# Kernel tuning notes

Hardware: AMD Instinct MI355X
Metric: run time of the kernel (lower is better)

The kernel has to match this reference:

```python
import jax, jax.numpy as jnp
import numpy as np

D = 256; NHEAD = 8; NQ = 300; NLAYERS = 6; NLEV = 3; NPTS = 4
DFF = 1024; NCLS = 80; BS = 16
SPATIAL = ((80, 80), (40, 40), (20, 20))
LM = sum(h * w for h, w in SPATIAL)
DH = D // NHEAD
PARAM_NAMES = ['sa_wq','sa_bq','sa_wk','sa_bk','sa_wv','sa_bv','sa_wo','sa_bo',
               'ln1_g','ln1_b','ln2_g','ln2_b','ln3_g','ln3_b',
               'off_w','off_b','attw_w','attw_b','val_w','val_b','out_w','out_b',
               'ffn_w1','ffn_b1','ffn_w2','ffn_b2',
               'bb_w1','bb_b1','bb_w2','bb_b2','bb_w3','bb_b3',
               'sc_w','sc_b','qp_w1','qp_b1','qp_w2','qp_b2']


def _ln(x, g, b, eps=1e-5):
    m = x.mean(-1, keepdims=True)
    v = ((x - m) ** 2).mean(-1, keepdims=True)
    return (x - m) * jax.lax.rsqrt(v + eps) * g + b


def _mlp2(x, w1, b1, w2, b2):
    # 2-layer MLP, ReLU on hidden only (act_final_layer=False)
    return jnp.maximum(x @ w1 + b1, 0.0) @ w2 + b2


def _inv_sigmoid(x, eps=1e-5):
    x = jnp.clip(x, 0.0, 1.0)
    return jnp.log(jnp.clip(x, eps, None) / jnp.clip(1.0 - x, eps, None))


def _mha(q, k, v, wq, bq, wk, bk, wv, bv, wo, bo):
    B, N, _ = q.shape
    Q = (q @ wq + bq).reshape(B, N, NHEAD, DH)
    K = (k @ wk + bk).reshape(B, N, NHEAD, DH)
    V = (v @ wv + bv).reshape(B, N, NHEAD, DH)
    att = jnp.einsum('bqhd,bkhd->bhqk', Q, K) * (1.0 / np.sqrt(DH))
    att = jax.nn.softmax(att, axis=-1)
    o = jnp.einsum('bhqk,bkhd->bqhd', att, V).reshape(B, N, D)
    return o @ wo + bo


def _bilinear(v, x, y, Hl, Wl):
    # v: [B, Hl*Wl, C]; x, y: [B, M] pixel coords (align_corners=False, zero padding)
    x0 = jnp.floor(x); y0 = jnp.floor(y)
    wx = x - x0; wy = y - y0
    out = 0.0
    for dx, dy, w in ((0, 0, (1 - wx) * (1 - wy)), (1, 0, wx * (1 - wy)),
                      (0, 1, (1 - wx) * wy), (1, 1, wx * wy)):
        xi = x0 + dx; yi = y0 + dy
        valid = (xi >= 0) & (xi < Wl) & (yi >= 0) & (yi < Hl)
        lin = (jnp.clip(yi, 0, Hl - 1) * Wl + jnp.clip(xi, 0, Wl - 1)).astype(jnp.int32)
        g = jnp.take_along_axis(v, lin[..., None], axis=1)
        out = out + g * (w * valid)[..., None]
    return out


def _deform_attn(q, ref, memory, ow, ob, aw, ab, vw, vb, pw, pb):
    # q: [B,NQ,D]; ref: [B,NQ,4] cxcywh in [0,1]; memory: [B,LM,D]
    B = q.shape[0]
    value = (memory @ vw + vb).reshape(B, LM, NHEAD, DH)
    off = (q @ ow + ob).reshape(B, NQ, NHEAD, NLEV, NPTS, 2)
    attw = jax.nn.softmax((q @ aw + ab).reshape(B, NQ, NHEAD, NLEV * NPTS), -1)
    attw = attw.reshape(B, NQ, NHEAD, NLEV, NPTS)
    r = ref[:, :, None, None, None, :]
    loc = r[..., :2] + off / NPTS * r[..., 2:] * 0.5  # [B,NQ,H,LV,P,2]
    start = 0
    acc = 0.0
    for lv, (Hl, Wl) in enumerate(SPATIAL):
        v = value[:, start:start + Hl * Wl]  # [B, Hl*Wl, H, DH]
        v = v.transpose(0, 2, 1, 3).reshape(B * NHEAD, Hl * Wl, DH)
        g = loc[:, :, :, lv]  # [B,NQ,H,P,2]
        x = (g[..., 0] * Wl - 0.5).transpose(0, 2, 1, 3).reshape(B * NHEAD, NQ * NPTS)
        y = (g[..., 1] * Hl - 0.5).transpose(0, 2, 1, 3).reshape(B * NHEAD, NQ * NPTS)
        s = _bilinear(v, x, y, Hl, Wl).reshape(B, NHEAD, NQ, NPTS, DH)
        w = attw[:, :, :, lv].transpose(0, 2, 1, 3)  # [B,H,NQ,P]
        acc = acc + (s * w[..., None]).sum(3)  # [B,H,NQ,DH]
        start += Hl * Wl
    o = acc.transpose(0, 2, 1, 3).reshape(B, NQ, D)
    return o @ pw + pb


def _decoder(tgt, ref_points_unact, memory, p):
    ref_d = jax.nn.sigmoid(ref_points_unact)
    out = tgt
    for i in range(NLAYERS):
        pos = _mlp2(ref_d, p['qp_w1'], p['qp_b1'], p['qp_w2'], p['qp_b2'])
        q = out + pos
        t2 = _mha(q, q, out, p['sa_wq'][i], p['sa_bq'][i], p['sa_wk'][i], p['sa_bk'][i],
                  p['sa_wv'][i], p['sa_bv'][i], p['sa_wo'][i], p['sa_bo'][i])
        out = _ln(out + t2, p['ln1_g'][i], p['ln1_b'][i])
        t2 = _deform_attn(out + pos, ref_d, memory, p['off_w'][i], p['off_b'][i],
                          p['attw_w'][i], p['attw_b'][i], p['val_w'][i], p['val_b'][i],
                          p['out_w'][i], p['out_b'][i])
        out = _ln(out + t2, p['ln2_g'][i], p['ln2_b'][i])
        out = _ln(out + _mlp2(out, p['ffn_w1'][i], p['ffn_b1'][i], p['ffn_w2'][i], p['ffn_b2'][i]),
                  p['ln3_g'][i], p['ln3_b'][i])
        h = jnp.maximum(out @ p['bb_w1'][i] + p['bb_b1'][i], 0.0)
        h = jnp.maximum(h @ p['bb_w2'][i] + p['bb_b2'][i], 0.0)
        delta = h @ p['bb_w3'][i] + p['bb_b3'][i]
        ref_d = jax.nn.sigmoid(delta + _inv_sigmoid(ref_d))
    logits = out @ p['sc_w'][NLAYERS - 1] + p['sc_b'][NLAYERS - 1]
    return ref_d, logits


def setup_inputs():
    key = jax.random.key(0)
    keys = iter(jax.random.split(key, 64))
    def rn(shape, s=0.02):
        return jax.random.normal(next(keys), shape, jnp.float32) * s
    L = NLAYERS
    inp = {
        'tgt': rn((BS, NQ, D), 1.0),
        'ref_points_unact': rn((BS, NQ, 4), 1.0),
        'memory': rn((BS, LM, D), 1.0),
    }
    for n in ['sa_wq', 'sa_wk', 'sa_wv', 'sa_wo', 'val_w', 'out_w', 'bb_w1', 'bb_w2']:
        inp[n] = rn((L, D, D))
    for n in ['sa_bq', 'sa_bk', 'sa_bv', 'sa_bo', 'ln1_b', 'ln2_b', 'ln3_b',
              'val_b', 'out_b', 'ffn_b2', 'bb_b1', 'bb_b2']:
        inp[n] = jnp.zeros((L, D), jnp.float32)
    for n in ['ln1_g', 'ln2_g', 'ln3_g']:
        inp[n] = jnp.ones((L, D), jnp.float32)
    OFF = NHEAD * NLEV * NPTS * 2
    ATT = NHEAD * NLEV * NPTS
    inp['off_w'] = rn((L, D, OFF)); inp['off_b'] = rn((L, OFF), 0.1)
    inp['attw_w'] = rn((L, D, ATT)); inp['attw_b'] = jnp.zeros((L, ATT), jnp.float32)
    inp['ffn_w1'] = rn((L, D, DFF)); inp['ffn_b1'] = jnp.zeros((L, DFF), jnp.float32)
    inp['ffn_w2'] = rn((L, DFF, D))
    inp['bb_w3'] = rn((L, D, 4)); inp['bb_b3'] = jnp.zeros((L, 4), jnp.float32)
    inp['sc_w'] = rn((L, D, NCLS)); inp['sc_b'] = jnp.zeros((L, NCLS), jnp.float32)
    inp['qp_w1'] = rn((4, 2 * D)); inp['qp_b1'] = jnp.zeros((2 * D,), jnp.float32)
    inp['qp_w2'] = rn((2 * D, D)); inp['qp_b2'] = jnp.zeros((D,), jnp.float32)
    return inp


def reference(tgt, ref_points_unact, memory, sa_wq, sa_bq, sa_wk, sa_bk, sa_wv, sa_bv,
              sa_wo, sa_bo, ln1_g, ln1_b, ln2_g, ln2_b, ln3_g, ln3_b, off_w, off_b,
              attw_w, attw_b, val_w, val_b, out_w, out_b, ffn_w1, ffn_b1, ffn_w2, ffn_b2,
              bb_w1, bb_b1, bb_w2, bb_b2, bb_w3, bb_b3, sc_w, sc_b,
              qp_w1, qp_b1, qp_w2, qp_b2):
    _a = dict(locals())
    p = {k: _a[k] for k in PARAM_NAMES}
    ref_d, logits = _decoder(tgt, ref_points_unact, memory, p)
    # eval path: stacked final-layer outputs, shape [1, BS, NQ, 4] and [1, BS, NQ, NCLS]
    return ref_d[None], logits[None]
```

## Files before the change

kernel.cpp:

```cpp
#include <hip/hip_runtime.h>
#include <hip/hip_bf16.h>

typedef __hip_bfloat16 bf16;
typedef short short8 __attribute__((ext_vector_type(8)));
typedef short short4v __attribute__((ext_vector_type(4)));
typedef float float4v __attribute__((ext_vector_type(4)));

#define D_ 256
#define NHEAD_ 8
#define DH_ 32
#define NQ_ 300
#define NLAYERS_ 6
#define DFF_ 1024
#define NCLS_ 80
#define BS_ 16
#define LM_ 8400
#define BN_ (BS_*NQ_)

static __device__ __forceinline__ short f2bf(float x){
    union{float f; unsigned u;} v; v.f = x;
    unsigned r = v.u + 0x7FFF + ((v.u>>16)&1);
    return (short)(r>>16);
}
static __device__ __forceinline__ float bf2f(short s){
    union{unsigned u; float f;} v; v.u = ((unsigned)(unsigned short)s)<<16; return v.f;
}

__global__ __launch_bounds__(256) void valproj_kernel(
    const short* __restrict__ memT, const short* __restrict__ WTall, size_t zWT,
    const float* __restrict__ vb, short* __restrict__ values)
{
    int m0 = blockIdx.x*64;
    int tid = threadIdx.x, lane = tid&63, wave = tid>>6;
    int wm = (wave>>1)*32, wn = (wave&1)*32;
    int lr = lane&15, lq = lane>>4;
    short8 af[2][8];
    #pragma unroll
    for(int t=0;t<8;t++){
        #pragma unroll
        for(int mi=0;mi<2;mi++)
            af[mi][t] = *(const short8*)(memT + (size_t)(m0+wm+mi*16+lr)*256 + t*32 + lq*8);
    }
    short8 pb[2][2];
    #pragma unroll
    for(int ni=0;ni<2;ni++)
        pb[0][ni] = *(const short8*)(WTall + (size_t)(wn+ni*16+lr)*256 + lq*8);
    for(int c=0;c<24;c++){
        int zi = c>>2;
        int n0 = (c&3)*64;
        float4v acc[2][2];
        #pragma unroll
        for(int i=0;i<2;i++)
            #pragma unroll
            for(int j=0;j<2;j++){ acc[i][j].x=0.f; acc[i][j].y=0.f; acc[i][j].z=0.f; acc[i][j].w=0.f; }
        const short* wz = WTall + (size_t)zi*zWT;
        #pragma unroll
        for(int t=0;t<8;t++){
            const int cur = t&1;
            if(t<7){
                #pragma unroll
                for(int ni=0;ni<2;ni++)
                    pb[cur^1][ni] = *(const short8*)(wz + (size_t)(n0+wn+ni*16+lr)*256 + (t+1)*32 + lq*8);
            } else if(c<23){
                int c2 = c+1; int zi2 = c2>>2; int n02 = (c2&3)*64;
                const short* wz2 = WTall + (size_t)zi2*zWT;
                #pragma unroll
                for(int ni=0;ni<2;ni++)
                    pb[cur^1][ni] = *(const short8*)(wz2 + (size_t)(n02+wn+ni*16+lr)*256 + lq*8);
            }
            acc[0][0] = __builtin_amdgcn_mfma_f32_16x16x32_bf16(af[0][t], pb[cur][0], acc[0][0], 0,0,0);
            acc[0][1] = __builtin_amdgcn_mfma_f32_16x16x32_bf16(af[0][t], pb[cur][1], acc[0][1], 0,0,0);
            acc[1][0] = __builtin_amdgcn_mfma_f32_16x16x32_bf16(af[1][t], pb[cur][0], acc[1][0], 0,0,0);
            acc[1][1] = __builtin_amdgcn_mfma_f32_16x16x32_bf16(af[1][t], pb[cur][1], acc[1][1], 0,0,0);
        }
        const float* bb = vb + (size_t)zi*256;
        bf16* out = (bf16*)values + (size_t)zi*((size_t)134400*256);
        #pragma unroll
        for(int mi=0;mi<2;mi++){
            #pragma unroll
            for(int rr=0;rr<4;rr++){
                int gm = m0+wm+mi*16+lq*4+rr;
                #pragma unroll
                for(int ni=0;ni<2;ni++){
                    int gn = n0+wn+ni*16+lr;
                    out[(size_t)gm*256+gn] = __float2bfloat16(acc[mi][ni][rr]+bb[gn]);
                }
            }
        }
    }
}

__global__ __launch_bounds__(256) void pos_mlp_kernel(
    const float* __restrict__ refd, const float* __restrict__ w1, const float* __restrict__ b1,
    const short* __restrict__ w2T, const float* __restrict__ b2, float* __restrict__ pos)
{
    __shared__ short hs[32*520];
    __shared__ float rs[32*4];
    int n0 = blockIdx.x*64, m0 = blockIdx.y*32;
    int tid = threadIdx.x;
    if(tid<128) rs[tid] = refd[(size_t)m0*4 + tid];
    __syncthreads();
    {
        int c0 = tid&255;
        float w1r[2][4], b1r[2];
        #pragma unroll
        for(int h=0;h<2;h++){
            int c = c0 + h*256;
            b1r[h] = b1[c];
            #pragma unroll
            for(int k=0;k<4;k++) w1r[h][k] = w1[k*512+c];
        }
        #pragma unroll 4
        for(int j=0;j<64;j++){
            int r = j>>1, h = j&1;
            int c = c0 + h*256;
            float v = 0.f;
            #pragma unroll
            for(int k=0;k<4;k++) v = fmaf(rs[r*4+k], w1r[h][k], v);
            v += b1r[h];
            hs[r*520+c] = f2bf(fmaxf(v,0.f));
        }
    }
    __syncthreads();
    int lane = tid&63, wave = tid>>6;
    int wm = (wave>>1)*16, wn = (wave&1)*32;
    int lr = lane&15, lq = lane>>4;
    float4v acc[2];
    #pragma unroll
    for(int j=0;j<2;j++){ acc[j].x=0.f; acc[j].y=0.f; acc[j].z=0.f; acc[j].w=0.f; }
    short8 pb[2][2];
    #pragma unroll
    for(int ni=0;ni<2;ni++)
        pb[0][ni] = *(const short8*)(w2T + (size_t)(n0+wn+ni*16+lr)*512 + lq*8);
    #pragma unroll
    for(int t=0;t<16;t++){
        const int cur = t&1;
        if(t<15){
            #pragma unroll
            for(int ni=0;ni<2;ni++)
                pb[cur^1][ni] = *(const short8*)(w2T + (size_t)(n0+wn+ni*16+lr)*512 + (t+1)*32 + lq*8);
        }
        short8 a0 = *(const short8*)(&hs[(wm+lr)*520 + t*32 + lq*8]);
        acc[0] = __builtin_amdgcn_mfma_f32_16x16x32_bf16(a0, pb[cur][0], acc[0], 0,0,0);
        acc[1] = __builtin_amdgcn_mfma_f32_16x16x32_bf16(a0, pb[cur][1], acc[1], 0,0,0);
    }
    #pragma unroll
    for(int rr=0;rr<4;rr++){
        int gm = m0+wm+lq*4+rr;
        #pragma unroll
        for(int ni=0;ni<2;ni++){
            int gn = n0+wn+ni*16+lr;
            pos[(size_t)gm*256+gn] = acc[ni][rr] + b2[gn];
        }
    }
}

#define LSTR 40

template<int TM, int TN, bool ABF16, bool RELU, bool OUTBF16>
__global__ __launch_bounds__(256) void mfma_gemm_kernel(
    const void* __restrict__ Av, const void* __restrict__ A2v,
    const void* __restrict__ A3v, int nA2lim,
    const short* __restrict__ WT, size_t zWT,
    const float* __restrict__ b0, const float* __restrict__ b1,
    const float* __restrict__ b2, int ns1, int ns2, size_t zB,
    void* __restrict__ Cv, size_t zC, int M, int K, int N, int nxt)
{
    __shared__ short As[2][TM*LSTR];
    __shared__ short Bs[2][TN*LSTR];
    int zz, n0;
    if(nxt){ zz = blockIdx.x / nxt; n0 = (blockIdx.x % nxt)*TN; }
    else   { zz = blockIdx.z;       n0 = blockIdx.x*TN; }
    WT += (size_t)zz*zWT; b0 += (size_t)zz*zB; b1 += (size_t)zz*zB; b2 += (size_t)zz*zB;
    int tid = threadIdx.x;
    int lane = tid&63, wave = tid>>6;
    int m0 = blockIdx.y*TM;
    const int MI = TM/32;
    const int NI = TN/32;
    int wm = (wave>>1)*(TM/2), wn = (wave&1)*(TN/2);
    int lr = lane&15, lq = lane>>4;
    float4v acc[MI][NI];
    #pragma unroll
    for(int i=0;i<MI;i++)
        #pragma unroll
        for(int j=0;j<NI;j++){ acc[i][j].x=0.f; acc[i][j].y=0.f; acc[i][j].z=0.f; acc[i][j].w=0.f; }

    const float* Af; const float* Ad; const short* Ah;
    if(ABF16){ Ah = (const short*)Av; Af=nullptr; Ad=nullptr; }
    else {
        Af = (n0 < nA2lim)? (const float*)Av : (const float*)A3v;
        Ad = (n0 < nA2lim)? (const float*)A2v : nullptr;
        Ah = nullptr;
    }

    short8  rA16[ABF16? TM/64 : 1];
    float4v rAf [ABF16? 1 : TM/32];
    float4v rAd [ABF16? 1 : TM/32];
    short8  rB[TN/64];

    auto LOAD = [&](int k0){
        if constexpr(ABF16){
            #pragma unroll
            for(int it=0; it<TM/64; ++it){
                int idx=(it*256+tid)*8; int r=idx>>5, kk=idx&31; int gm=m0+r;
                short8 v = {};
                if(gm<M) v = *(const short8*)(Ah + (size_t)gm*K + (k0+kk));
                rA16[it]=v;
            }
        } else {
            #pragma unroll
            for(int it=0; it<TM/32; ++it){
                int idx=(it*256+tid)*4; int r=idx>>5, kk=idx&31; int gm=m0+r;
                float4v v; v.x=0.f;v.y=0.f;v.z=0.f;v.w=0.f;
                float4v w; w.x=0.f;w.y=0.f;w.z=0.f;w.w=0.f;
                if(gm<M){
                    v = *(const float4v*)(Af + (size_t)gm*K + (k0+kk));
                    if(Ad) w = *(const float4v*)(Ad + (size_t)gm*K + (k0+kk));
                }
                rAf[it]=v; rAd[it]=w;
            }
        }
        #pragma unroll
        for(int it=0; it<TN/64; ++it){
            int idx=(it*256+tid)*8; int r=idx>>5, kk=idx&31; int gn=n0+r;
            short8 v = {};
            if(gn<N) v = *(const short8*)(WT + (size_t)gn*K + (k0+kk));
            rB[it]=v;
        }
    };
    auto STORE = [&](int buf){
        if constexpr(ABF16){
            #pragma unroll
            for(int it=0; it<TM/64; ++it){
                int idx=(it*256+tid)*8; int r=idx>>5, kk=idx&31;
                *(short8*)(&As[buf][r*LSTR+kk]) = rA16[it];
            }
        } else {
            #pragma unroll
            for(int it=0; it<TM/32; ++it){
                int idx=(it*256+tid)*4; int r=idx>>5, kk=idx&31;
                float4v v = rAf[it];
                if(Ad){ v.x+=rAd[it].x; v.y+=rAd[it].y; v.z+=rAd[it].z; v.w+=rAd[it].w; }
                short4v h; h.x=f2bf(v.x); h.y=f2bf(v.y); h.z=f2bf(v.z); h.w=f2bf(v.w);
                *(short4v*)(&As[buf][r*LSTR+kk]) = h;
            }
        }
        #pragma unroll
        for(int it=0; it<TN/64; ++it){
            int idx=(it*256+tid)*8; int r=idx>>5, kk=idx&31;
            *(short8*)(&Bs[buf][r*LSTR+kk]) = rB[it];
        }
    };

    const int nt = K>>5;
    LOAD(0);
    STORE(0);
    __syncthreads();
    for(int t=0; t<nt; ++t){
        int cb = t&1;
        if(t+1<nt) LOAD((t+1)<<5);
        short8 af[MI], bfr[NI];
        #pragma unroll
        for(int mi=0;mi<MI;mi++) af[mi]  = *(const short8*)(&As[cb][(wm+mi*16+lr)*LSTR + lq*8]);
        #pragma unroll
        for(int ni=0;ni<NI;ni++) bfr[ni] = *(const short8*)(&Bs[cb][(wn+ni*16+lr)*LSTR + lq*8]);
        #pragma unroll
        for(int mi=0;mi<MI;mi++)
            #pragma unroll
            for(int ni=0;ni<NI;ni++)
                acc[mi][ni] = __builtin_amdgcn_mfma_f32_16x16x32_bf16(af[mi], bfr[ni], acc[mi][ni], 0,0,0);
        if(t+1<nt){
            STORE(cb^1);
            __syncthreads();
        }
    }
    float* Cf=(float*)Cv + (size_t)zz*zC; bf16* Ch=(bf16*)Cv + (size_t)zz*zC;
    #pragma unroll
    for(int mi=0;mi<MI;mi++){
        #pragma unroll
        for(int r=0;r<4;r++){
            int gm = m0+wm+mi*16+lq*4+r;
            if(gm>=M) continue;
            #pragma unroll
            for(int ni=0;ni<NI;ni++){
                int gn = n0+wn+ni*16+lr;
                if(gn>=N) continue;
                float bv = (gn<ns1)? b0[gn] : ((gn<ns2)? b1[gn-ns1] : b2[gn-ns2]);
                float v = acc[mi][ni][r] + bv;
                if(RELU) v = fmaxf(v,0.f);
                if(OUTBF16) Ch[(size_t)gm*N+gn]=__float2bfloat16(v);
                else        Cf[(size_t)gm*N+gn]=v;
            }
        }
    }
}

__global__ __launch_bounds__(256) void fused_mha_kernel(
    const float* __restrict__ QKV, short* __restrict__ O)
{
    const int ld = 768;
    int bh = blockIdx.y; int b = bh>>3, h = bh&7;
    int q0 = blockIdx.x*64;
    __shared__ short lds[31104];
    short* Vts = lds;
    short* Qs  = lds + 10368;
    short* Ks  = lds + 12672;
    short* Ps  = lds + 10368;
    int tid = threadIdx.x;
    for(int idx=tid; idx<64*8; idx+=256){
        int r=idx>>3, c4=(idx&7)*4; int gq=q0+r;
        float4v v; v.x=0.f;v.y=0.f;v.z=0.f;v.w=0.f;
        if(gq<NQ_) v = *(const float4v*)(QKV + ((size_t)(b*NQ_+gq))*ld + h*DH_ + c4);
        short4v h4; h4.x=f2bf(v.x);h4.y=f2bf(v.y);h4.z=f2bf(v.z);h4.w=f2bf(v.w);
        *(short4v*)(Qs + r*36 + c4) = h4;
    }
    for(int idx=tid; idx<304*8; idx+=256){
        int r=idx>>3, c4=(idx&7)*4;
        float4v v; v.x=0.f;v.y=0.f;v.z=0.f;v.w=0.f;
        if(r<NQ_) v = *(const float4v*)(QKV + 256 + ((size_t)(b*NQ_+r))*ld + h*DH_ + c4);
        short4v h4; h4.x=f2bf(v.x);h4.y=f2bf(v.y);h4.z=f2bf(v.z);h4.w=f2bf(v.w);
        *(short4v*)(Ks + r*36 + c4) = h4;
    }
    for(int idx=tid; idx<320*8; idx+=256){
        int r=idx>>3, c4=(idx&7)*4;
        float4v v; v.x=0.f;v.y=0.f;v.z=0.f;v.w=0.f;
        if(r<NQ_) v = *(const float4v*)(QKV + 512 + ((size_t)(b*NQ_+r))*ld + h*DH_ + c4);
        Vts[(c4+0)*324+r]=f2bf(v.x); Vts[(c4+1)*324+r]=f2bf(v.y);
        Vts[(c4+2)*324+r]=f2bf(v.z); Vts[(c4+3)*324+r]=f2bf(v.w);
    }
    __syncthreads();

    int lane = tid&63, wave = tid>>6;
    int lr = lane&15, lq = lane>>4;
    int mrow = wave*16;
    const float scale = 0.17677669529663687f;

    float4v acc[19];
    #pragma unroll
    for(int t=0;t<19;t++){ acc[t].x=0.f; acc[t].y=0.f; acc[t].z=0.f; acc[t].w=0.f; }
    short8 afrag = *(const short8*)(&Qs[(mrow+lr)*36 + lq*8]);
    #pragma unroll
    for(int t=0;t<19;t++){
        short8 bfrag = *(const short8*)(&Ks[(t*16+lr)*36 + lq*8]);
        acc[t] = __builtin_amdgcn_mfma_f32_16x16x32_bf16(afrag, bfrag, acc[t], 0,0,0);
    }
    __syncthreads();

    for(int idx=tid; idx<64*16; idx+=256){
        int r=idx>>4, c=idx&15;
        Ps[r*324 + 304 + c]=0;
    }
    #pragma unroll
    for(int t=0;t<19;t++){
        #pragma unroll
        for(int r=0;r<4;r++) acc[t][r] *= scale;
    }
    if(lr>=12){
        #pragma unroll
        for(int r=0;r<4;r++) acc[18][r] = -1e30f;
    }
    float mx[4];
    #pragma unroll
    for(int r=0;r<4;r++){
        float m = acc[0][r];
        #pragma unroll
        for(int t=1;t<19;t++) m = fmaxf(m, acc[t][r]);
        m = fmaxf(m, __shfl_xor(m,1)); m = fmaxf(m, __shfl_xor(m,2));
        m = fmaxf(m, __shfl_xor(m,4)); m = fmaxf(m, __shfl_xor(m,8));
        mx[r]=m;
    }
    float sum[4] = {0.f,0.f,0.f,0.f};
    #pragma unroll
    for(int t=0;t<19;t++){
        #pragma unroll
        for(int r=0;r<4;r++){
            float p = __expf(acc[t][r]-mx[r]);
            acc[t][r]=p; sum[r]+=p;
        }
    }
    #pragma unroll
    for(int r=0;r<4;r++){
        float s = sum[r];
        s += __shfl_xor(s,1); s += __shfl_xor(s,2);
        s += __shfl_xor(s,4); s += __shfl_xor(s,8);
        sum[r] = 1.f/s;
    }
    #pragma unroll
    for(int t=0;t<19;t++){
        #pragma unroll
        for(int r=0;r<4;r++){
            Ps[(mrow + lq*4 + r)*324 + t*16 + lr] = f2bf(acc[t][r]*sum[r]);
        }
    }
    __syncthreads();
    float4v oacc[2];
    oacc[0].x=0.f;oacc[0].y=0.f;oacc[0].z=0.f;oacc[0].w=0.f;
    oacc[1]=oacc[0];
    #pragma unroll
    for(int kc=0;kc<10;kc++){
        short8 pa = *(const short8*)(&Ps[(mrow+lr)*324 + kc*32 + lq*8]);
        #pragma unroll
        for(int n=0;n<2;n++){
            short8 vb = *(const short8*)(&Vts[(n*16+lr)*324 + kc*32 + lq*8]);
            oacc[n] = __builtin_amdgcn_mfma_f32_16x16x32_bf16(pa, vb, oacc[n], 0,0,0);
        }
    }
    #pragma unroll
    for(int n=0;n<2;n++){
        #pragma unroll
        for(int r=0;r<4;r++){
            int gq = q0 + mrow + lq*4 + r;
            if(gq<NQ_)
                O[((size_t)(b*NQ_+gq))*D_ + h*DH_ + n*16 + lr] = f2bf(oacc[n][r]);
        }
    }
}

#define NTD 74
struct TD { const float* src; unsigned dstoff; int K, N, base; };
struct TAll { TD d[NTD]; };

__global__ __launch_bounds__(256) void transpose_all_kernel(TAll p, short* __restrict__ WTb){
    int blk = blockIdx.x;
    int di = 0;
    #pragma unroll 1
    for(int i=0;i<NTD;i++){ if(blk >= p.d[i].base) di = i; }
    TD d = p.d[di];
    int rel = blk - d.base;
    int ntx = (d.N+31)/32;
    int tn = (rel % ntx)*32, tk = (rel / ntx)*32;
    __shared__ float t[32][33];
    int tx = threadIdx.x&31, ty = threadIdx.x>>5;
    for(int i=0;i<32;i+=8){
        int k = tk+ty+i, n = tn+tx;
        t[ty+i][tx] = (k<d.K && n<d.N)? d.src[(size_t)k*d.N+n] : 0.f;
    }
    __syncthreads();
    short* out = WTb + d.dstoff;
    for(int i=0;i<32;i+=8){
        int n = tn+ty+i, k = tk+tx;
        if(n<d.N && k<d.K) out[(size_t)n*d.K+k] = f2bf(t[tx][ty+i]);
    }
}

template<bool RELU, bool BBOX>
__global__ __launch_bounds__(256) void gemm_kernel(
    const float* __restrict__ A, const float* __restrict__ W,
    const float* __restrict__ bias, float* __restrict__ Cf,
    int M, int K, int N)
{
    __shared__ float As[16][68];
    __shared__ float Bs[16][68];
    int tid = threadIdx.x;
    int m0 = blockIdx.y*64, n0 = blockIdx.x*64;
    int tm = tid>>4, tn = tid&15;
    float acc[4][4] = {};
    int lam = tid>>2;
    int lak = (tid&3)*4;
    int lbk = tid>>4;
    int lbn = (tid&15)*4;
    for(int k0=0;k0<K;k0+=16){
        {
            int m = m0+lam;
            #pragma unroll
            for(int j=0;j<4;j++){
                int k = k0+lak+j;
                float v=0.f;
                if(m<M && k<K) v = A[(size_t)m*K+k];
                As[lak+j][lam]=v;
            }
        }
        {
            int k = k0+lbk;
            #pragma unroll
            for(int j=0;j<4;j++){
                int n = n0+lbn+j;
                float v=0.f;
                if(k<K && n<N) v = W[(size_t)k*N+n];
                Bs[lbk][lbn+j]=v;
            }
        }
        __syncthreads();
        #pragma unroll
        for(int kk=0;kk<16;kk++){
            float a[4], bb[4];
            #pragma unroll
            for(int i=0;i<4;i++) a[i]=As[kk][tm*4+i];
            #pragma unroll
            for(int j=0;j<4;j++) bb[j]=Bs[kk][tn*4+j];
            #pragma unroll
            for(int i=0;i<4;i++)
                #pragma unroll
                for(int j=0;j<4;j++) acc[i][j] += a[i]*bb[j];
        }
        __syncthreads();
    }
    #pragma unroll
    for(int i=0;i<4;i++){
        int m=m0+tm*4+i; if(m>=M) continue;
        #pragma unroll
        for(int j=0;j<4;j++){
            int n=n0+tn*4+j; if(n>=N) continue;
            float v = acc[i][j] + bias[n];
            if(BBOX){
                float x = Cf[(size_t)m*N+n];
                x = fminf(fmaxf(x,0.f),1.f);
                float num = fmaxf(x,1e-5f), den = fmaxf(1.f-x,1e-5f);
                float nd = v + logf(num/den);
                Cf[(size_t)m*N+n] = 1.f/(1.f+expf(-nd));
            } else {
                if(RELU) v = fmaxf(v,0.f);
                Cf[(size_t)m*N+n]=v;
            }
        }
    }
}

__global__ void copy_kernel(const float* __restrict__ a, float* __restrict__ o, int n){
    int i = blockIdx.x*blockDim.x+threadIdx.x;
    if(i<n) o[i]=a[i];
}
__global__ void cvt_f32_bf16_kernel(const float* __restrict__ a, short* __restrict__ o, int n4){
    int i = blockIdx.x*blockDim.x+threadIdx.x;
    if(i<n4){
        float4v v = *(const float4v*)(a + (size_t)i*4);
        short4v h; h.x=f2bf(v.x); h.y=f2bf(v.y); h.z=f2bf(v.z); h.w=f2bf(v.w);
        *(short4v*)(o + (size_t)i*4) = h;
    }
}
__global__ void sigmoid_init_kernel(const float* __restrict__ a, float* __restrict__ o, int n){
    int i = blockIdx.x*blockDim.x+threadIdx.x;
    if(i<n){ float x=a[i]; o[i]=1.f/(1.f+expf(-x)); }
}
__global__ void write_out_kernel(const float* __restrict__ refd, const float* __restrict__ logits, float* __restrict__ out){
    int i = blockIdx.x*blockDim.x+threadIdx.x;
    if(i<BN_*4) out[i]=refd[i];
    else if(i<BN_*4+BN_*NCLS_) out[i]=logits[i-BN_*4];
}

__global__ __launch_bounds__(256) void ln_residual_kernel(
    float* __restrict__ cur, const short* __restrict__ t2b,
    const float* __restrict__ g, const float* __restrict__ b,
    short* __restrict__ cb)
{
    int row = blockIdx.x; int c = threadIdx.x;
    size_t idx = (size_t)row*D_+c;
    float x = cur[idx] + bf2f(t2b[idx]);
    float v1 = x, v2 = x*x;
    #pragma unroll
    for(int o=32;o>0;o>>=1){ v1 += __shfl_down(v1,o,64); v2 += __shfl_down(v2,o,64); }
    __shared__ float s1[4], s2[4], st[2];
    int wid=c>>6, lane=c&63;
    if(lane==0){ s1[wid]=v1; s2[wid]=v2; }
    __syncthreads();
    if(c==0){
        float a=0,d=0;
        #pragma unroll
        for(int i=0;i<4;i++){a+=s1[i]; d+=s2[i];}
        st[0]=a/(float)D_; st[1]=d/(float)D_;
    }
    __syncthreads();
    float m=st[0], var=st[1]-m*m;
    float y = (x-m)*rsqrtf(var+1e-5f)*g[c] + b[c];
    cur[idx]=y;
    if(cb) cb[idx]=f2bf(y);
}

__global__ __launch_bounds__(256) void deform_sample_kernel(
    const float* __restrict__ refd, const float* __restrict__ oab,
    const bf16* __restrict__ value, short* __restrict__ outacc)
{
    int row = blockIdx.x; int b = row/NQ_;
    int tid = threadIdx.x; int h = tid>>5, c = tid&31;
    __shared__ float so[192], sa[96], sr[4];
    if(tid<192) so[tid]=oab[(size_t)row*288+tid];
    if(tid<96)  sa[tid]=oab[(size_t)row*288+192+tid];
    if(tid<4)   sr[tid]=refd[(size_t)row*4+tid];
    __syncthreads();
    if(tid<8){
        float* p = sa + tid*12;
        float m=-1e30f;
        #pragma unroll
        for(int i2=0;i2<12;i2++) m=fmaxf(m,p[i2]);
        float s=0.f;
        #pragma unroll
        for(int i2=0;i2<12;i2++){ float e=__expf(p[i2]-m); p[i2]=e; s+=e; }
        float inv=1.f/s;
        #pragma unroll
        for(int i2=0;i2<12;i2++) p[i2]*=inv;
    }
    __syncthreads();
    float cx=sr[0], cy=sr[1], rw=sr[2], rh=sr[3];
    const int HS[3]={80,40,20}, WS[3]={80,40,20}, ST[3]={0,6400,8000};
    float acc=0.f;
    const bf16* vb = value + (size_t)b*LM_*D_ + h*DH_ + c;
    for(int lv=0;lv<3;lv++){
        int Hl=HS[lv], Wl=WS[lv], st=ST[lv];
        #pragma unroll
        for(int pt=0;pt<4;pt++){
            int oi = ((h*3+lv)*4+pt)*2;
            float ox=so[oi], oy=so[oi+1];
            float wa=sa[h*12+lv*4+pt];
            float lx = cx + ox*0.25f*rw*0.5f;
            float ly = cy + oy*0.25f*rh*0.5f;
            float x = lx*(float)Wl - 0.5f, y = ly*(float)Hl - 0.5f;
            float x0f=floorf(x), y0f=floorf(y);
            float wx=x-x0f, wy=y-y0f;
            int x0=(int)x0f, y0=(int)y0f;
            #pragma unroll
            for(int dy=0;dy<2;dy++){
                #pragma unroll
                for(int dx=0;dx<2;dx++){
                    int xi=x0+dx, yi=y0+dy;
                    if(xi>=0 && xi<Wl && yi>=0 && yi<Hl){
                        float w = (dx? wx : 1.f-wx)*(dy? wy : 1.f-wy);
                        int lin = yi*Wl+xi;
                        acc += __bfloat162float(vb[(size_t)(st+lin)*D_]) * (w*wa);
                    }
                }
            }
        }
    }
    outacc[(size_t)row*D_+tid]=f2bf(acc);
}

static void gemm_bbox(const float*A, const float*W, const float*b, float*refd,
                      int M,int K,int N, hipStream_t s){
    dim3 g((N+63)/64,(M+63)/64);
    gemm_kernel<false,true><<<g,256,0,s>>>(A,W,b,refd,M,K,N);
}
static void g64x(const void*A, const void*A2, const void*A3, int nA2lim,
                 const short*WT, const float*b0, const float*b1, const float*b2,
                 int ns1, int ns2, void*C, int M,int K,int N,
                 bool abf16, bool relu, bool outbf, hipStream_t s){
    dim3 g((N+63)/64,(M+63)/64,1);
    #define CALLG(AB,RL,OB) mfma_gemm_kernel<64,64,AB,RL,OB><<<g,256,0,s>>>(A,A2,A3,nA2lim,WT,0,b0,b1,b2,ns1,ns2,0,C,0,M,K,N,0)
    if(abf16){
        if(relu){ if(outbf) CALLG(true,true,true);  else CALLG(true,true,false); }
        else    { if(outbf) CALLG(true,false,true); else CALLG(true,false,false); }
    } else {
        if(relu){ if(outbf) CALLG(false,true,true);  else CALLG(false,true,false); }
        else    { if(outbf) CALLG(false,false,true); else CALLG(false,false,false); }
    }
    #undef CALLG
}
static void g64(const float*A, const float*A2, const float*A3, int nA2lim,
                const short*WT, const float*b0, const float*b1, const float*b2,
                int ns1, int ns2, void*C, int M,int K,int N,
                bool relu, bool outbf, hipStream_t s){
    g64x(A,A2,A3,nA2lim,WT,b0,b1,b2,ns1,ns2,C,M,K,N,false,relu,outbf,s);
}
static void g64b(const short*A, const short*WT, const float*b, void*C,
                 int M,int K,int N, hipStream_t s){
    g64x(A,nullptr,nullptr,1<<30,WT,b,b,b,N,N+1,C,M,K,N,true,false,true,s);
}
static int ntiles(int K,int N){ return ((N+31)/32)*((K+31)/32); }

extern "C" void kernel_launch(void* const* d_in, const int* in_sizes, int n_in,
                              void* d_out, int out_size, void* d_ws, size_t ws_size,
                              hipStream_t stream) {
    const float* tgt   = (const float*)d_in[0];
    const float* rpu   = (const float*)d_in[1];
    const float* mem   = (const float*)d_in[2];
    const float* sa_wq = (const float*)d_in[3];
    const float* sa_wk = (const float*)d_in[4];
    const float* sa_wv = (const float*)d_in[5];
    const float* sa_wo = (const float*)d_in[6];
    const float* val_w = (const float*)d_in[7];
    const float* out_w = (const float*)d_in[8];
    const float* bb_w1 = (const float*)d_in[9];
    const float* bb_w2 = (const float*)d_in[10];
    const float* sa_bq = (const float*)d_in[11];
    const float* sa_bk = (const float*)d_in[12];
    const float* sa_bv = (const float*)d_in[13];
    const float* sa_bo = (const float*)d_in[14];
    const float* ln1_b = (const float*)d_in[15];
    const float* ln2_b = (const float*)d_in[16];
    const float* ln3_b = (const float*)d_in[17];
    const float* val_b = (const float*)d_in[18];
    const float* out_b = (const float*)d_in[19];
    const float* ffn_b2= (const float*)d_in[20];
    const float* bb_b1 = (const float*)d_in[21];
    const float* bb_b2 = (const float*)d_in[22];
    const float* ln1_g = (const float*)d_in[23];
    const float* ln2_g = (const float*)d_in[24];
    const float* ln3_g = (const float*)d_in[25];
    const float* off_w = (const float*)d_in[26];
    const float* off_b = (const float*)d_in[27];
    const float* attw_w= (const float*)d_in[28];
    const float* attw_b= (const float*)d_in[29];
    const float* ffn_w1= (const float*)d_in[30];
    const float* ffn_b1= (const float*)d_in[31];
    const float* ffn_w2= (const float*)d_in[32];
    const float* bb_w3 = (const float*)d_in[33];
    const float* bb_b3 = (const float*)d_in[34];
    const float* sc_w  = (const float*)d_in[35];
    const float* sc_b  = (const float*)d_in[36];
    const float* qp_w1 = (const float*)d_in[37];
    const float* qp_b1 = (const float*)d_in[38];
    const float* qp_w2 = (const float*)d_in[39];
    const float* qp_b2 = (const float*)d_in[40];

    const size_t BND = (size_t)BN_*D_;
    const size_t USZ = (size_t)BN_*DFF_;
    const size_t LMD = (size_t)BS_*LM_*D_;
    const size_t LSZ = 1122304;

    float* ws   = (float*)d_ws;
    float* cur  = ws;
    float* pos  = cur + BND;
    float* refd = pos + BND;
    float* U    = refd + (size_t)BN_*4;
    short* tmp16 = (short*)(U + USZ);
    short* t216  = tmp16 + BND;
    short* WT    = t216 + BND;
    short* qp2T  = WT + 6*LSZ;
    short* scT   = qp2T + 131072;
    short* X     = scT + 20480;
    float* QKVh   = U;
    float* offsb  = U;
    short* ffnh16 = (short*)U;
    short* bb1b   = (short*)U;
    float* bb2    = U + BND;
    float* logitsb= U;
    short* curb = tmp16;

    size_t offX = (size_t)((char*)X - (char*)d_ws);
    int vmode;
    if(ws_size >= offX + 7*LMD*2)      vmode = 3;
    else if(ws_size >= offX + 6*LMD*2) vmode = 2;
    else if(ws_size >= offX + 4*LMD)   vmode = 1;
    else                               vmode = 0;
    short* memT   = X;
    short* values = (vmode==3)? X + LMD : X;
    short* value1 = X + LMD;
    short* value0 = X;

    const int nBN_D = (int)BND;
    copy_kernel<<<(nBN_D+255)/256,256,0,stream>>>(tgt, cur, nBN_D);
    sigmoid_init_kernel<<<(BN_*4+255)/256,256,0,stream>>>(rpu, refd, BN_*4);
    if(vmode==1 || vmode==3){
        int n4 = (int)(LMD/4);
        cvt_f32_bf16_kernel<<<(n4+255)/256,256,0,stream>>>(mem, memT, n4);
    }

    {
        TAll tp; int base=0; int di=0;
        const size_t offs[12] = { 0,65536,131072,196608,262144,327680,
                                  393216,442368,466944,729088,991232,1056768 };
        const int Ks[12] = { 256,256,256,256,256,256,256,256,256,1024,256,256 };
        const int Ns[12] = { 256,256,256,256,256,256,192,96,1024,256,256,256 };
        for(int l=0;l<NLAYERS_;l++){
            const float* srcs[12] = { sa_wq+(size_t)l*D_*D_, sa_wk+(size_t)l*D_*D_, sa_wv+(size_t)l*D_*D_,
                                      sa_wo+(size_t)l*D_*D_, val_w+(size_t)l*D_*D_, out_w+(size_t)l*D_*D_,
                                      off_w+(size_t)l*D_*192, attw_w+(size_t)l*D_*96,
                                      ffn_w1+(size_t)l*D_*DFF_, ffn_w2+(size_t)l*DFF_*D_,
                                      bb_w1+(size_t)l*D_*D_, bb_w2+(size_t)l*D_*D_ };
            for(int j=0;j<12;j++){
                tp.d[di] = { srcs[j], (unsigned)(l*LSZ + offs[j]), Ks[j], Ns[j], base };
                base += ntiles(Ks[j],Ns[j]); di++;
            }
        }
        tp.d[di] = { qp_w2, (unsigned)(6*LSZ), 512, 256, base }; base += ntiles(512,256); di++;
        tp.d[di] = { sc_w + (size_t)(NLAYERS_-1)*D_*NCLS_, (unsigned)(6*LSZ+131072), 256, 80, base }; base += ntiles(256,80); di++;
        transpose_all_kernel<<<base,256,0,stream>>>(tp, WT);
    }

    if(vmode==3){
        valproj_kernel<<<2100,256,0,stream>>>(memT, WT+262144, LSZ, val_b, values);
    } else if(vmode==2){
        dim3 g(12,1050,1);
        mfma_gemm_kernel<128,128,false,false,true><<<g,256,0,stream>>>(
            mem,nullptr,mem,1<<30, WT+262144, LSZ,
            val_b,val_b,val_b, 256,257, 256, values, LMD, BS_*LM_, D_, D_, 2);
    }

    for(int i=0;i<NLAYERS_;i++){
        const bf16* value_i;
        if(vmode>=2) value_i = (const bf16*)(values + (size_t)i*LMD);
        else {
            dim3 g(2,1050,1);
            if(vmode==1){
                mfma_gemm_kernel<128,128,true,false,true><<<g,256,0,stream>>>(
                    memT,nullptr,nullptr,1<<30, WT+i*LSZ+262144, 0,
                    val_b+(size_t)i*D_,val_b,val_b, 256,257, 0, value1, 0, BS_*LM_, D_, D_, 0);
                value_i = (const bf16*)value1;
            } else {
                mfma_gemm_kernel<128,128,false,false,true><<<g,256,0,stream>>>(
                    mem,nullptr,mem,1<<30, WT+i*LSZ+262144, 0,
                    val_b+(size_t)i*D_,val_b,val_b, 256,257, 0, value0, 0, BS_*LM_, D_, D_, 0);
                value_i = (const bf16*)value0;
            }
        }
        pos_mlp_kernel<<<dim3(4,150),256,0,stream>>>(refd, qp_w1, qp_b1, qp2T, qp_b2, pos);
        g64(cur, pos, cur, 512, WT+i*LSZ,
            sa_bq+(size_t)i*D_, sa_bk+(size_t)i*D_, sa_bv+(size_t)i*D_, 256, 512,
            QKVh, BN_, D_, 768, false,false, stream);
        {
            dim3 g((NQ_+63)/64, BS_*NHEAD_);
            fused_mha_kernel<<<g,256,0,stream>>>(QKVh, tmp16);
        }
        g64b(tmp16, WT+i*LSZ+196608, sa_bo+(size_t)i*D_, t216, BN_, D_, D_, stream);
        ln_residual_kernel<<<BN_,256,0,stream>>>(cur, t216, ln1_g+(size_t)i*D_, ln1_b+(size_t)i*D_, nullptr);
        g64(cur, pos, cur, 1<<30, WT+i*LSZ+393216,
            off_b+(size_t)i*192, attw_b+(size_t)i*96, attw_b+(size_t)i*96, 192, 288,
            offsb, BN_, D_, 288, false,false, stream);
        deform_sample_kernel<<<BN_,256,0,stream>>>(refd, offsb, value_i, tmp16);
        g64b(tmp16, WT+i*LSZ+327680, out_b+(size_t)i*D_, t216, BN_, D_, D_, stream);
        ln_residual_kernel<<<BN_,256,0,stream>>>(cur, t216, ln2_g+(size_t)i*D_, ln2_b+(size_t)i*D_, curb);
        g64x(curb,nullptr,nullptr,1<<30, WT+i*LSZ+466944, ffn_b1+(size_t)i*DFF_,ffn_b1,ffn_b1, DFF_,DFF_+1,
             ffnh16, BN_, D_, DFF_, true,true,true, stream);
        g64x(ffnh16,nullptr,nullptr,1<<30, WT+i*LSZ+729088, ffn_b2+(size_t)i*D_,ffn_b2,ffn_b2, 256,257,
             t216, BN_, DFF_, D_, true,false,true, stream);
        ln_residual_kernel<<<BN_,256,0,stream>>>(cur, t216, ln3_g+(size_t)i*D_, ln3_b+(size_t)i*D_, curb);
        g64x(curb,nullptr,nullptr,1<<30, WT+i*LSZ+991232, bb_b1+(size_t)i*D_,bb_b1,bb_b1, 256,257,
             bb1b, BN_, D_, D_, true,true,true, stream);
        g64x(bb1b,nullptr,nullptr,1<<30, WT+i*LSZ+1056768, bb_b2+(size_t)i*D_,bb_b2,bb_b2, 256,257,
             bb2, BN_, D_, D_, true,true,false, stream);
        gemm_bbox(bb2, bb_w3+(size_t)i*D_*4, bb_b3+(size_t)i*4, refd, BN_, D_, 4, stream);
    }
    g64x(curb,nullptr,nullptr,1<<30, scT, sc_b+(size_t)(NLAYERS_-1)*NCLS_,sc_b,sc_b, NCLS_,NCLS_+1,
         logitsb, BN_, D_, NCLS_, true,false,false, stream);
    int tot = BN_*4 + BN_*NCLS_;
    write_out_kernel<<<(tot+255)/256,256,0,stream>>>(refd, logitsb, (float*)d_out);
}
```

Baseline: 2.428 ms.

## Fuse bbox MLP head into single MFMA kernel and swap value projection kernel

Replaces the three-launch bbox head (two bf16 MFMA GEMMs plus a scalar fp32 GEMM with the sigmoid/inverse-sigmoid refinement) with one kernel. Each 16-row block keeps its hidden activations in shared memory and does the 256->4 projection and reference-point update in place. This removes two intermediate global round trips and two launches per layer. Separately, when vmode is 3 the custom value-projection kernel is replaced by the generic templated MFMA GEMM, and the dead valproj and scalar gemm kernels are deleted. The fused kernel runs only 300 blocks, and every wave re-reads the weight tiles straight from global memory, so occupancy and weight reuse may be limited.

```diff
diff --git a/kernel.cpp b/kernel.cpp
--- a/kernel.cpp
+++ b/kernel.cpp
@@ -26,66 +26,83 @@
     union{unsigned u; float f;} v; v.u = ((unsigned)(unsigned short)s)<<16; return v.f;
 }
 
-__global__ __launch_bounds__(256) void valproj_kernel(
-    const short* __restrict__ memT, const short* __restrict__ WTall, size_t zWT,
-    const float* __restrict__ vb, short* __restrict__ values)
+__global__ __launch_bounds__(256) void bbox_head_kernel(
+    const short* __restrict__ curb,
+    const short* __restrict__ w1T, const float* __restrict__ b1,
+    const short* __restrict__ w2T, const float* __restrict__ b2,
+    const float* __restrict__ w3, const float* __restrict__ b3,
+    float* __restrict__ refd)
 {
-    int m0 = blockIdx.x*64;
+    __shared__ short h1[16*264];
+    __shared__ float h2[16*260];
+    int m0 = blockIdx.x*16;
     int tid = threadIdx.x, lane = tid&63, wave = tid>>6;
-    int wm = (wave>>1)*32, wn = (wave&1)*32;
     int lr = lane&15, lq = lane>>4;
-    short8 af[2][8];
-    #pragma unroll
-    for(int t=0;t<8;t++){
-        #pragma unroll
-        for(int mi=0;mi<2;mi++)
-            af[mi][t] = *(const short8*)(memT + (size_t)(m0+wm+mi*16+lr)*256 + t*32 + lq*8);
-    }
-    short8 pb[2][2];
-    #pragma unroll
-    for(int ni=0;ni<2;ni++)
-        pb[0][ni] = *(const short8*)(WTall + (size_t)(wn+ni*16+lr)*256 + lq*8);
-    for(int c=0;c<24;c++){
-        int zi = c>>2;
-        int n0 = (c&3)*64;
-        float4v acc[2][2];
-        #pragma unroll
-        for(int i=0;i<2;i++)
-            #pragma unroll
-            for(int j=0;j<2;j++){ acc[i][j].x=0.f; acc[i][j].y=0.f; acc[i][j].z=0.f; acc[i][j].w=0.f; }
-        const short* wz = WTall + (size_t)zi*zWT;
-        #pragma unroll
-        for(int t=0;t<8;t++){
-            const int cur = t&1;
-            if(t<7){
-                #pragma unroll
-                for(int ni=0;ni<2;ni++)
-                    pb[cur^1][ni] = *(const short8*)(wz + (size_t)(n0+wn+ni*16+lr)*256 + (t+1)*32 + lq*8);
-            } else if(c<23){
-                int c2 = c+1; int zi2 = c2>>2; int n02 = (c2&3)*64;
-                const short* wz2 = WTall + (size_t)zi2*zWT;
-                #pragma unroll
-                for(int ni=0;ni<2;ni++)
-                    pb[cur^1][ni] = *(const short8*)(wz2 + (size_t)(n02+wn+ni*16+lr)*256 + lq*8);
-            }
-            acc[0][0] = __builtin_amdgcn_mfma_f32_16x16x32_bf16(af[0][t], pb[cur][0], acc[0][0], 0,0,0);
-            acc[0][1] = __builtin_amdgcn_mfma_f32_16x16x32_bf16(af[0][t], pb[cur][1], acc[0][1], 0,0,0);
-            acc[1][0] = __builtin_amdgcn_mfma_f32_16x16x32_bf16(af[1][t], pb[cur][0], acc[1][0], 0,0,0);
-            acc[1][1] = __builtin_amdgcn_mfma_f32_16x16x32_bf16(af[1][t], pb[cur][1], acc[1][1], 0,0,0);
-        }
-        const float* bb = vb + (size_t)zi*256;
-        bf16* out = (bf16*)values + (size_t)zi*((size_t)134400*256);
-        #pragma unroll
-        for(int mi=0;mi<2;mi++){
-            #pragma unroll
-            for(int rr=0;rr<4;rr++){
-                int gm = m0+wm+mi*16+lq*4+rr;
-                #pragma unroll
-                for(int ni=0;ni<2;ni++){
-                    int gn = n0+wn+ni*16+lr;
-                    out[(size_t)gm*256+gn] = __float2bfloat16(acc[mi][ni][rr]+bb[gn]);
-                }
-            }
+    int n0 = wave*64;
+    short8 af[8];
+    #pragma unroll
+    for(int kt=0;kt<8;kt++)
+        af[kt] = *(const short8*)(curb + (size_t)(m0+lr)*256 + kt*32 + lq*8);
+    float4v acc[4];
+    #pragma unroll
+    for(int nf=0;nf<4;nf++){ acc[nf].x=0.f; acc[nf].y=0.f; acc[nf].z=0.f; acc[nf].w=0.f; }
+    #pragma unroll
+    for(int kt=0;kt<8;kt++){
+        #pragma unroll
+        for(int nf=0;nf<4;nf++){
+            short8 bfr = *(const short8*)(w1T + (size_t)(n0+nf*16+lr)*256 + kt*32 + lq*8);
+            acc[nf] = __builtin_amdgcn_mfma_f32_16x16x32_bf16(af[kt], bfr, acc[nf], 0,0,0);
+        }
+    }
+    #pragma unroll
+    for(int nf=0;nf<4;nf++){
+        #pragma unroll
+        for(int rr=0;rr<4;rr++){
+            int row = lq*4+rr, gn = n0+nf*16+lr;
+            float v = acc[nf][rr] + b1[gn];
+            v = fmaxf(v,0.f);
+            ((bf16*)h1)[row*264+gn] = __float2bfloat16(v);
+        }
+    }
+    __syncthreads();
+    #pragma unroll
+    for(int nf=0;nf<4;nf++){ acc[nf].x=0.f; acc[nf].y=0.f; acc[nf].z=0.f; acc[nf].w=0.f; }
+    #pragma unroll
+    for(int kt=0;kt<8;kt++){
+        short8 a2 = *(const short8*)(&h1[lr*264 + kt*32 + lq*8]);
+        #pragma unroll
+        for(int nf=0;nf<4;nf++){
+            short8 bfr = *(const short8*)(w2T + (size_t)(n0+nf*16+lr)*256 + kt*32 + lq*8);
+            acc[nf] = __builtin_amdgcn_mfma_f32_16x16x32_bf16(a2, bfr, acc[nf], 0,0,0);
+        }
+    }
+    #pragma unroll
+    for(int nf=0;nf<4;nf++){
+        #pragma unroll
+        for(int rr=0;rr<4;rr++){
+            int row = lq*4+rr, gn = n0+nf*16+lr;
+            float v = acc[nf][rr] + b2[gn];
+            h2[row*260+gn] = fmaxf(v,0.f);
+        }
+    }
+    __syncthreads();
+    {
+        int row = tid>>4, sub = tid&15;
+        int n = sub>>2, kq = sub&3;
+        float p = 0.f;
+        const float* hr = h2 + row*260 + kq*64;
+        #pragma unroll
+        for(int k=0;k<64;k++) p = fmaf(hr[k], w3[(kq*64+k)*4+n], p);
+        p += __shfl_xor(p,1);
+        p += __shfl_xor(p,2);
+        if(kq==0){
+            float delta = p + b3[n];
+            size_t idx = (size_t)(m0+row)*4+n;
+            float x = refd[idx];
+            x = fminf(fmaxf(x,0.f),1.f);
+            float num = fmaxf(x,1e-5f), den = fmaxf(1.f-x,1e-5f);
+            float nd = delta + logf(num/den);
+            refd[idx] = 1.f/(1.f+expf(-nd));
         }
     }
 }
@@ -443,79 +460,6 @@
     }
 }
 
-template<bool RELU, bool BBOX>
-__global__ __launch_bounds__(256) void gemm_kernel(
-    const float* __restrict__ A, const float* __restrict__ W,
-    const float* __restrict__ bias, float* __restrict__ Cf,
-    int M, int K, int N)
-{
-    __shared__ float As[16][68];
-    __shared__ float Bs[16][68];
-    int tid = threadIdx.x;
-    int m0 = blockIdx.y*64, n0 = blockIdx.x*64;
-    int tm = tid>>4, tn = tid&15;
-    float acc[4][4] = {};
-    int lam = tid>>2;
-    int lak = (tid&3)*4;
-    int lbk = tid>>4;
-    int lbn = (tid&15)*4;
-    for(int k0=0;k0<K;k0+=16){
-        {
-            int m = m0+lam;
-            #pragma unroll
-            for(int j=0;j<4;j++){
-                int k = k0+lak+j;
-                float v=0.f;
-                if(m<M && k<K) v = A[(size_t)m*K+k];
-                As[lak+j][lam]=v;
-            }
-        }
-        {
-            int k = k0+lbk;
-            #pragma unroll
-            for(int j=0;j<4;j++){
-                int n = n0+lbn+j;
-                float v=0.f;
-                if(k<K && n<N) v = W[(size_t)k*N+n];
-                Bs[lbk][lbn+j]=v;
-            }
-        }
-        __syncthreads();
-        #pragma unroll
-        for(int kk=0;kk<16;kk++){
-            float a[4], bb[4];
-            #pragma unroll
-            for(int i=0;i<4;i++) a[i]=As[kk][tm*4+i];
-            #pragma unroll
-            for(int j=0;j<4;j++) bb[j]=Bs[kk][tn*4+j];
-            #pragma unroll
-            for(int i=0;i<4;i++)
-                #pragma unroll
-                for(int j=0;j<4;j++) acc[i][j] += a[i]*bb[j];
-        }
-        __syncthreads();
-    }
-    #pragma unroll
-    for(int i=0;i<4;i++){
-        int m=m0+tm*4+i; if(m>=M) continue;
-        #pragma unroll
-        for(int j=0;j<4;j++){
-            int n=n0+tn*4+j; if(n>=N) continue;
-            float v = acc[i][j] + bias[n];
-            if(BBOX){
-                float x = Cf[(size_t)m*N+n];
-                x = fminf(fmaxf(x,0.f),1.f);
-                float num = fmaxf(x,1e-5f), den = fmaxf(1.f-x,1e-5f);
-                float nd = v + logf(num/den);
-                Cf[(size_t)m*N+n] = 1.f/(1.f+expf(-nd));
-            } else {
-                if(RELU) v = fmaxf(v,0.f);
-                Cf[(size_t)m*N+n]=v;
-            }
-        }
-    }
-}
-
 __global__ void copy_kernel(const float* __restrict__ a, float* __restrict__ o, int n){
     int i = blockIdx.x*blockDim.x+threadIdx.x;
     if(i<n) o[i]=a[i];
@@ -624,11 +568,6 @@
     outacc[(size_t)row*D_+tid]=f2bf(acc);
 }
 
-static void gemm_bbox(const float*A, const float*W, const float*b, float*refd,
-                      int M,int K,int N, hipStream_t s){
-    dim3 g((N+63)/64,(M+63)/64);
-    gemm_kernel<false,true><<<g,256,0,s>>>(A,W,b,refd,M,K,N);
-}
 static void g64x(const void*A, const void*A2, const void*A3, int nA2lim,
                  const short*WT, const float*b0, const float*b1, const float*b2,
                  int ns1, int ns2, void*C, int M,int K,int N,
@@ -720,8 +659,6 @@
     float* QKVh   = U;
     float* offsb  = U;
     short* ffnh16 = (short*)U;
-    short* bb1b   = (short*)U;
-    float* bb2    = U + BND;
     float* logitsb= U;
     short* curb = tmp16;
 
@@ -767,7 +704,10 @@
     }
 
     if(vmode==3){
-        valproj_kernel<<<2100,256,0,stream>>>(memT, WT+262144, LSZ, val_b, values);
+        dim3 g(12,1050,1);
+        mfma_gemm_kernel<128,128,true,false,true><<<g,256,0,stream>>>(
+            memT,nullptr,nullptr,1<<30, WT+262144, LSZ,
+            val_b,val_b,val_b, 256,257, 256, values, LMD, BS_*LM_, D_, D_, 2);
     } else if(vmode==2){
         dim3 g(12,1050,1);
         mfma_gemm_kernel<128,128,false,false,true><<<g,256,0,stream>>>(
@@ -813,11 +753,10 @@
         g64x(ffnh16,nullptr,nullptr,1<<30, WT+i*LSZ+729088, ffn_b2+(size_t)i*D_,ffn_b2,ffn_b2, 256,257,
              t216, BN_, DFF_, D_, true,false,true, stream);
         ln_residual_kernel<<<BN_,256,0,stream>>>(cur, t216, ln3_g+(size_t)i*D_, ln3_b+(size_t)i*D_, curb);
-        g64x(curb,nullptr,nullptr,1<<30, WT+i*LSZ+991232, bb_b1+(size_t)i*D_,bb_b1,bb_b1, 256,257,
-             bb1b, BN_, D_, D_, true,true,true, stream);
-        g64x(bb1b,nullptr,nullptr,1<<30, WT+i*LSZ+1056768, bb_b2+(size_t)i*D_,bb_b2,bb_b2, 256,257,
-             bb2, BN_, D_, D_, true,true,false, stream);
-        gemm_bbox(bb2, bb_w3+(size_t)i*D_*4, bb_b3+(size_t)i*4, refd, BN_, D_, 4, stream);
+        bbox_head_kernel<<<BN_/16,256,0,stream>>>(curb,
+            WT+i*LSZ+991232, bb_b1+(size_t)i*D_,
+            WT+i*LSZ+1056768, bb_b2+(size_t)i*D_,
+            bb_w3+(size_t)i*D_*4, bb_b3+(size_t)i*4, refd);
     }
     g64x(curb,nullptr,nullptr,1<<30, scT, sc_b+(size_t)(NLAYERS_-1)*NCLS_,sc_b,sc_b, NCLS_,NCLS_+1,
          logitsb, BN_, D_, NCLS_, true,false,false, stream);
```

After: 2.167 ms. -10.8%, faster.
